# Kernel tuning notes

Measured on AMD Instinct MI355X. Metric: run time of the kernel, lower is better.

Reference implementation:

```python
import jax, jax.numpy as jnp
import numpy as np

B, SC, SV = 32, 300, 300
D, H, L, E, F = 512, 8, 6, 6, 1024
SEM = 768
VF = SEM + 1 + 1 + 6  # semantic + scene_offset + motion + emotion(6) = 776
CHORD, ROOT, ATTR = 159, 14, 14


def _ln(x, g, b, eps=1e-5):
    m = x.mean(-1, keepdims=True)
    v = ((x - m) ** 2).mean(-1, keepdims=True)
    return (x - m) / jnp.sqrt(v + eps) * g + b


def _mha(q_in, kv_in, qkv_w, qkv_b, ow, ob, mask=None):
    d = q_in.shape[-1]
    hd = d // H
    q = (q_in @ qkv_w[:d].T + qkv_b[:d]).reshape(q_in.shape[0], q_in.shape[1], H, hd)
    k = (kv_in @ qkv_w[d:2 * d].T + qkv_b[d:2 * d]).reshape(kv_in.shape[0], kv_in.shape[1], H, hd)
    v = (kv_in @ qkv_w[2 * d:].T + qkv_b[2 * d:]).reshape(kv_in.shape[0], kv_in.shape[1], H, hd)
    s = jnp.einsum('bqhd,bkhd->bhqk', q, k) / jnp.sqrt(jnp.asarray(hd, q.dtype))
    if mask is not None:
        s = s + mask
    a = jax.nn.softmax(s, axis=-1)
    o = jnp.einsum('bhqk,bkhd->bqhd', a, v).reshape(q_in.shape)
    return o @ ow.T + ob


def _moe(x, gw, gb, w1, b1, w2, b2, w3, b3):
    # top-2 routing over E experts, SwiGLU experts (GLUExpert)
    probs = jax.nn.softmax(x @ gw.T + gb, axis=-1)  # [B,S,E]
    topv, topi = jax.lax.top_k(probs, 2)
    wts = topv / topv.sum(-1, keepdims=True)
    full = (jax.nn.one_hot(topi, E, dtype=x.dtype) * wts[..., None]).sum(-2)  # [B,S,E]
    h = jax.nn.silu(jnp.einsum('bsd,edf->bsef', x, w1) + b1) * (jnp.einsum('bsd,edf->bsef', x, w2) + b2)
    eo = jnp.einsum('bsef,efd->bsed', h, w3) + b3
    return jnp.einsum('bse,bsed->bsd', full, eo)


def reference(x, x_root, x_attr, fsem, fkey, fscene, fmotion, femotion, emb_root, emb_attr, w_chord, b_chord, w_vis, b_vis, pos_c, pos_v, enc_qkv_w, enc_qkv_b, enc_ow, enc_ob, enc_ln1_g, enc_ln1_b, enc_ln2_g, enc_ln2_b, enc_gw, enc_gb, enc_w1, enc_b1, enc_w2, enc_b2, enc_w3, enc_b3, enc_fg, enc_fb, dec_sqkv_w, dec_sqkv_b, dec_sow, dec_sob, dec_cqkv_w, dec_cqkv_b, dec_cow, dec_cob, dec_ln1_g, dec_ln1_b, dec_ln2_g, dec_ln2_b, dec_ln3_g, dec_ln3_b, dec_gw, dec_gb, dec_w1, dec_b1, dec_w2, dec_b2, dec_w3, dec_b3, dec_fg, dec_fb, wout, bout):
    Bq, S = x_root.shape
    xe = emb_root[x_root] + emb_attr[x_attr]  # chord root + attr embeddings
    keyp = jnp.broadcast_to(fkey[:, 0][:, None, None], (Bq, S, 1)).astype(xe.dtype)
    xf = jnp.concatenate([xe, keyp], -1) @ w_chord.T + b_chord
    vfc = jnp.concatenate([fsem, fscene[..., None], fmotion[..., None], femotion], -1)  # [B,Sv,VF]
    vf = vfc @ w_vis.T + b_vis
    xf = xf + pos_c[:S][None]
    vf = vf + pos_v[:vf.shape[1]][None]
    causal = jnp.where(jnp.tril(jnp.ones((S, S), bool)), 0.0, jnp.finfo(xf.dtype).min).astype(xf.dtype)
    # encoder (post-norm): self-attn -> add&norm -> MoE -> add&norm
    h = vf
    for i in range(L):
        a = _mha(h, h, enc_qkv_w[i], enc_qkv_b[i], enc_ow[i], enc_ob[i])
        h = _ln(h + a, enc_ln1_g[i], enc_ln1_b[i])
        m = _moe(h, enc_gw[i], enc_gb[i], enc_w1[i], enc_b1[i], enc_w2[i], enc_b2[i], enc_w3[i], enc_b3[i])
        h = _ln(h + m, enc_ln2_g[i], enc_ln2_b[i])
    mem = _ln(h, enc_fg, enc_fb)
    # decoder: masked self-attn, cross-attn, MoE, each add&norm
    h = xf
    for i in range(L):
        a = _mha(h, h, dec_sqkv_w[i], dec_sqkv_b[i], dec_sow[i], dec_sob[i], causal)
        h = _ln(h + a, dec_ln1_g[i], dec_ln1_b[i])
        c = _mha(h, mem, dec_cqkv_w[i], dec_cqkv_b[i], dec_cow[i], dec_cob[i])
        h = _ln(h + c, dec_ln2_g[i], dec_ln2_b[i])
        m = _moe(h, dec_gw[i], dec_gb[i], dec_w1[i], dec_b1[i], dec_w2[i], dec_b2[i], dec_w3[i], dec_b3[i])
        h = _ln(h + m, dec_ln3_g[i], dec_ln3_b[i])
    h = _ln(h, dec_fg, dec_fb)
    return h @ wout.T + bout


def setup_inputs():
    key = jax.random.key(0)
    ks = iter(jax.random.split(key, 256))
    def nrm(*s):
        return jax.random.normal(next(ks), s, jnp.float32) * 0.02
    d = {}
    d['x'] = jax.random.randint(next(ks), (B, SC), 0, CHORD)
    d['x_root'] = jax.random.randint(next(ks), (B, SC), 0, ROOT)
    d['x_attr'] = jax.random.randint(next(ks), (B, SC), 0, ATTR)
    d['fsem'] = jax.random.normal(next(ks), (B, SV, SEM), jnp.float32)
    d['fkey'] = jax.random.uniform(next(ks), (B, 1), jnp.float32)
    d['fscene'] = jax.random.uniform(next(ks), (B, SV), jnp.float32)
    d['fmotion'] = jax.random.uniform(next(ks), (B, SV), jnp.float32)
    d['femotion'] = jax.random.uniform(next(ks), (B, SV, 6), jnp.float32)
    d['emb_root'] = nrm(ROOT, D)
    d['emb_attr'] = nrm(ATTR, D)
    d['w_chord'] = nrm(D, D + 1)
    d['b_chord'] = jnp.zeros((D,), jnp.float32)
    d['w_vis'] = nrm(D, VF)
    d['b_vis'] = jnp.zeros((D,), jnp.float32)
    d['pos_c'] = nrm(SC, D)
    d['pos_v'] = nrm(SV, D)
    def attn_params(pfx_qkv, pfx_o):
        d[pfx_qkv + '_w'] = nrm(L, 3 * D, D)
        d[pfx_qkv + '_b'] = jnp.zeros((L, 3 * D), jnp.float32)
        d[pfx_o + 'w'] = nrm(L, D, D)
        d[pfx_o + 'b'] = jnp.zeros((L, D), jnp.float32)
    attn_params('enc_qkv', 'enc_o')
    attn_params('dec_sqkv', 'dec_so')
    attn_params('dec_cqkv', 'dec_co')
    def moe_params(pfx):
        d[pfx + 'gw'] = nrm(L, E, D)
        d[pfx + 'gb'] = jnp.zeros((L, E), jnp.float32)
        d[pfx + 'w1'] = nrm(L, E, D, F)
        d[pfx + 'b1'] = jnp.zeros((L, E, F), jnp.float32)
        d[pfx + 'w2'] = nrm(L, E, D, F)
        d[pfx + 'b2'] = jnp.zeros((L, E, F), jnp.float32)
        d[pfx + 'w3'] = nrm(L, E, F, D)
        d[pfx + 'b3'] = jnp.zeros((L, E, D), jnp.float32)
    moe_params('enc_')
    moe_params('dec_')
    for n in ['enc_ln1', 'enc_ln2', 'dec_ln1', 'dec_ln2', 'dec_ln3']:
        d[n + '_g'] = jnp.ones((L, D), jnp.float32)
        d[n + '_b'] = jnp.zeros((L, D), jnp.float32)
    d['enc_fg'] = jnp.ones((D,), jnp.float32)
    d['enc_fb'] = jnp.zeros((D,), jnp.float32)
    d['dec_fg'] = jnp.ones((D,), jnp.float32)
    d['dec_fb'] = jnp.zeros((D,), jnp.float32)
    d['wout'] = nrm(CHORD, D)
    d['bout'] = jnp.zeros((CHORD,), jnp.float32)
    return d
```

## Files before the change

### kernel.cpp

```cpp
#include <hip/hip_runtime.h>

constexpr int B_ = 32, S_ = 300, D_ = 512, H_ = 8;
constexpr int L_ = 6, E_ = 6, F_ = 1024;
constexpr int CHORD_ = 159;
constexpr int R_ = B_ * S_;
constexpr int TD_ = 3 * D_;
constexpr int MT_ = R_ / 64;
constexpr size_t WSCAP_ = (size_t)E_ * F_ * 512;

typedef short bfrag __attribute__((ext_vector_type(8)));
typedef float facc  __attribute__((ext_vector_type(4)));

static __device__ __forceinline__ facc mfma_(bfrag a, bfrag b, facc c) {
    return __builtin_amdgcn_mfma_f32_16x16x32_bf16(a, b, c, 0, 0, 0);
}

static __device__ __forceinline__ short f2bf_rne(float f) {
    unsigned u = __float_as_uint(f);
    return (short)((u + 0x7FFFu + ((u >> 16) & 1u)) >> 16);
}
static __device__ __forceinline__ void split2(float x, short& hi, short& lo) {
    unsigned u = __float_as_uint(x);
    hi = (short)(u >> 16);
    float fh = __uint_as_float(u & 0xFFFF0000u);
    lo = f2bf_rne(x - fh);
}

static __device__ __forceinline__ float2 blockReduce2(float s, float ss) {
    __shared__ float red[4][2];
    #pragma unroll
    for (int o = 32; o > 0; o >>= 1) { s += __shfl_down(s, o); ss += __shfl_down(ss, o); }
    const int wid = threadIdx.x >> 6, lane = threadIdx.x & 63;
    if (lane == 0) { red[wid][0] = s; red[wid][1] = ss; }
    __syncthreads();
    if (threadIdx.x == 0) {
        for (int w = 1; w < 4; ++w) { s += red[w][0]; ss += red[w][1]; }
        red[0][0] = s; red[0][1] = ss;
    }
    __syncthreads();
    return make_float2(red[0][0], red[0][1]);
}

__global__ void wsplit_kern(const float* __restrict__ src, short* __restrict__ dh, short* __restrict__ dl,
                            int N, int K, int Kp)
{
    const int idx = blockIdx.x * 256 + threadIdx.x;
    if (idx >= N * Kp) return;
    const int n = idx / Kp, k = idx - n * Kp;
    const float v = (k < K) ? src[(size_t)n * K + k] : 0.f;
    short sh, sl; split2(v, sh, sl);
    dh[idx] = sh; dl[idx] = sl;
}

__global__ __launch_bounds__(256) void tsplit_kern(const float* __restrict__ src,
                                                   short* __restrict__ dh, short* __restrict__ dl,
                                                   int K, int N)
{
    __shared__ float tile[32][33];
    const size_t eo = (size_t)blockIdx.z * K * N;
    const float* s = src + eo;
    short* oh = dh + eo;
    short* ol = dl + eo;
    const int kb = blockIdx.x * 32, nb = blockIdx.y * 32;
    const int c = threadIdx.x & 31, r0 = threadIdx.x >> 5;
    #pragma unroll
    for (int p = 0; p < 4; ++p) {
        const int r = r0 + p * 8;
        tile[r][c] = s[(size_t)(kb + r) * N + nb + c];
    }
    __syncthreads();
    #pragma unroll
    for (int p = 0; p < 4; ++p) {
        const int wn = r0 + p * 8;
        const float v = tile[c][wn];
        short sh, sl; split2(v, sh, sl);
        const size_t o = (size_t)(nb + wn) * K + kb + c;
        oh[o] = sh; ol[o] = sl;
    }
}

__global__ __launch_bounds__(128) void gemm_mfma(
    const short* __restrict__ Xh, const short* __restrict__ Xl,
    const short* __restrict__ Wh, const short* __restrict__ Wl, int Kp,
    const float* __restrict__ bias, const float* __restrict__ pos,
    float* __restrict__ Y, int ldy, int N,
    short* __restrict__ Yh, short* __restrict__ Yl)
{
    __shared__ __align__(16) short Ah[64][40], Al[64][40];
    __shared__ __align__(16) short Bh[128][40], Bl[128][40];
    const int m0 = blockIdx.x * 64, n0 = blockIdx.y * 128;
    const int tid = threadIdx.x;
    const int w = tid >> 6, l = tid & 63;
    const facc zero = {0.f, 0.f, 0.f, 0.f};
    facc acc[4][4];
    #pragma unroll
    for (int i = 0; i < 4; ++i)
        #pragma unroll
        for (int j = 0; j < 4; ++j) acc[i][j] = zero;
    const int ar = tid >> 2, aks = (tid & 3) * 8;
    const int bcol = tid;
    const bool bok = (n0 + bcol) < N;
    const size_t bbase = (size_t)(n0 + bcol) * Kp;
    const bfrag zf = {0, 0, 0, 0, 0, 0, 0, 0};
    for (int kc = 0; kc < Kp; kc += 32) {
        #pragma unroll
        for (int p = 0; p < 2; ++p) {
            const int row = ar + p * 32;
            const size_t go = (size_t)(m0 + row) * Kp + kc + aks;
            *(bfrag*)&Ah[row][aks] = *(const bfrag*)&Xh[go];
            *(bfrag*)&Al[row][aks] = *(const bfrag*)&Xl[go];
        }
        if (bok) {
            #pragma unroll
            for (int i2 = 0; i2 < 4; ++i2) {
                *(bfrag*)&Bh[bcol][i2 * 8] = *(const bfrag*)&Wh[bbase + kc + i2 * 8];
                *(bfrag*)&Bl[bcol][i2 * 8] = *(const bfrag*)&Wl[bbase + kc + i2 * 8];
            }
        } else {
            #pragma unroll
            for (int i2 = 0; i2 < 4; ++i2) {
                *(bfrag*)&Bh[bcol][i2 * 8] = zf;
                *(bfrag*)&Bl[bcol][i2 * 8] = zf;
            }
        }
        __syncthreads();
        bfrag ah[4], al[4];
        #pragma unroll
        for (int i2 = 0; i2 < 4; ++i2) {
            ah[i2] = *(const bfrag*)&Ah[i2 * 16 + (l & 15)][(l >> 4) * 8];
            al[i2] = *(const bfrag*)&Al[i2 * 16 + (l & 15)][(l >> 4) * 8];
        }
        #pragma unroll
        for (int j = 0; j < 4; ++j) {
            const int cc = w * 64 + j * 16 + (l & 15);
            const bfrag bh = *(const bfrag*)&Bh[cc][(l >> 4) * 8];
            const bfrag bl = *(const bfrag*)&Bl[cc][(l >> 4) * 8];
            #pragma unroll
            for (int i2 = 0; i2 < 4; ++i2) {
                acc[i2][j] = mfma_(ah[i2], bh, acc[i2][j]);
                acc[i2][j] = mfma_(al[i2], bh, acc[i2][j]);
                acc[i2][j] = mfma_(ah[i2], bl, acc[i2][j]);
            }
        }
        __syncthreads();
    }
    #pragma unroll
    for (int i2 = 0; i2 < 4; ++i2) {
        #pragma unroll
        for (int r = 0; r < 4; ++r) {
            const int m = m0 + i2 * 16 + (l >> 4) * 4 + r;
            #pragma unroll
            for (int j = 0; j < 4; ++j) {
                const int n = n0 + w * 64 + j * 16 + (l & 15);
                if (n < N) {
                    float y = acc[i2][j][r];
                    if (bias) y += bias[n];
                    if (pos)  y += pos[(size_t)(m % S_) * N + n];
                    Y[(size_t)m * ldy + n] = y;
                    if (Yh) {
                        short sh, sl; split2(y, sh, sl);
                        Yh[(size_t)m * ldy + n] = sh;
                        Yl[(size_t)m * ldy + n] = sl;
                    }
                }
            }
        }
    }
}

template<bool CAUSAL>
__global__ __launch_bounds__(320) void attn_kern(const float* __restrict__ qkv,
                                                 short* __restrict__ oh, short* __restrict__ ol)
{
    __shared__ float Ks[64][64];
    __shared__ float Vs[64][64];
    const int b = blockIdx.x >> 3, hh = blockIdx.x & 7;
    const int tid = threadIdx.x;
    const float* base = qkv + (size_t)b * S_ * TD_ + hh * 64;
    const bool act = tid < S_;
    float4 q4[16];
    if (act) {
        const float4* qp = (const float4*)(base + (size_t)tid * TD_);
        #pragma unroll
        for (int dd = 0; dd < 16; ++dd) q4[dd] = qp[dd];
    }
    float m = -3.0e38f, lsum = 0.f;
    float acc[64];
    #pragma unroll
    for (int d = 0; d < 64; ++d) acc[d] = 0.f;
    for (int j0 = 0; j0 < S_; j0 += 64) {
        const int tn = min(64, S_ - j0);
        __syncthreads();
        for (int idx = tid; idx < 64 * 64; idx += 320) {
            const int jj = idx >> 6, d = idx & 63;
            const bool ok = jj < tn;
            Ks[jj][d] = ok ? base[(size_t)(j0 + jj) * TD_ + D_ + d] : 0.f;
            Vs[jj][d] = ok ? base[(size_t)(j0 + jj) * TD_ + 2 * D_ + d] : 0.f;
        }
        __syncthreads();
        if (act) {
            const int jmax = CAUSAL ? min(tn, tid - j0 + 1) : tn;
            for (int jj = 0; jj < jmax; ++jj) {
                const float4* kp = (const float4*)Ks[jj];
                float s = 0.f;
                #pragma unroll
                for (int dd = 0; dd < 16; ++dd) {
                    const float4 kv = kp[dd];
                    s += q4[dd].x * kv.x + q4[dd].y * kv.y + q4[dd].z * kv.z + q4[dd].w * kv.w;
                }
                s *= 0.125f;
                float p;
                if (s > m) {
                    const float r = __expf(m - s);
                    lsum *= r;
                    #pragma unroll
                    for (int d = 0; d < 64; ++d) acc[d] *= r;
                    m = s; p = 1.f;
                } else {
                    p = __expf(s - m);
                }
                lsum += p;
                const float4* vp = (const float4*)Vs[jj];
                #pragma unroll
                for (int dd = 0; dd < 16; ++dd) {
                    const float4 vv = vp[dd];
                    acc[dd * 4 + 0] += p * vv.x; acc[dd * 4 + 1] += p * vv.y;
                    acc[dd * 4 + 2] += p * vv.z; acc[dd * 4 + 3] += p * vv.w;
                }
            }
        }
    }
    if (act) {
        const float inv = 1.f / lsum;
        const size_t ob = (size_t)(b * S_ + tid) * D_ + hh * 64;
        #pragma unroll
        for (int d = 0; d < 64; ++d) {
            short sh, sl; split2(acc[d] * inv, sh, sl);
            oh[ob + d] = sh; ol[ob + d] = sl;
        }
    }
}

__global__ __launch_bounds__(256) void add_ln_kern(float* __restrict__ h, const float* __restrict__ a,
    const float* __restrict__ g, const float* __restrict__ bb,
    short* __restrict__ dh, short* __restrict__ dl)
{
    const int r = blockIdx.x, tid = threadIdx.x;
    const size_t off = (size_t)r * D_;
    const float x0 = h[off + tid] + a[off + tid];
    const float x1 = h[off + tid + 256] + a[off + tid + 256];
    const float2 red = blockReduce2(x0 + x1, x0 * x0 + x1 * x1);
    const float mean = red.x * (1.f / D_);
    const float var = red.y * (1.f / D_) - mean * mean;
    const float rs = rsqrtf(var + 1e-5f);
    const float y0 = (x0 - mean) * rs * g[tid] + bb[tid];
    const float y1 = (x1 - mean) * rs * g[tid + 256] + bb[tid + 256];
    h[off + tid] = y0; h[off + tid + 256] = y1;
    short sh, sl;
    split2(y0, sh, sl); dh[off + tid] = sh;       dl[off + tid] = sl;
    split2(y1, sh, sl); dh[off + tid + 256] = sh; dl[off + tid + 256] = sl;
}

__global__ __launch_bounds__(256) void add2_ln_kern(float* __restrict__ h, const float* __restrict__ moeout,
    const float* __restrict__ g, const float* __restrict__ bb,
    short* __restrict__ dh, short* __restrict__ dl)
{
    const int r = blockIdx.x, tid = threadIdx.x;
    const size_t off = (size_t)r * D_;
    const size_t m0 = (size_t)(2 * r) * D_, m1 = (size_t)(2 * r + 1) * D_;
    const float x0 = h[off + tid]       + moeout[m0 + tid]       + moeout[m1 + tid];
    const float x1 = h[off + tid + 256] + moeout[m0 + tid + 256] + moeout[m1 + tid + 256];
    const float2 red = blockReduce2(x0 + x1, x0 * x0 + x1 * x1);
    const float mean = red.x * (1.f / D_);
    const float var = red.y * (1.f / D_) - mean * mean;
    const float rs = rsqrtf(var + 1e-5f);
    const float y0 = (x0 - mean) * rs * g[tid] + bb[tid];
    const float y1 = (x1 - mean) * rs * g[tid + 256] + bb[tid + 256];
    h[off + tid] = y0; h[off + tid + 256] = y1;
    short sh, sl;
    split2(y0, sh, sl); dh[off + tid] = sh;       dl[off + tid] = sl;
    split2(y1, sh, sl); dh[off + tid + 256] = sh; dl[off + tid + 256] = sl;
}

__global__ __launch_bounds__(256) void ln_kern(const float* __restrict__ src,
    const float* __restrict__ g, const float* __restrict__ bb,
    short* __restrict__ dh, short* __restrict__ dl)
{
    const int r = blockIdx.x, tid = threadIdx.x;
    const size_t off = (size_t)r * D_;
    const float x0 = src[off + tid];
    const float x1 = src[off + tid + 256];
    const float2 red = blockReduce2(x0 + x1, x0 * x0 + x1 * x1);
    const float mean = red.x * (1.f / D_);
    const float var = red.y * (1.f / D_) - mean * mean;
    const float rs = rsqrtf(var + 1e-5f);
    const float y0 = (x0 - mean) * rs * g[tid] + bb[tid];
    const float y1 = (x1 - mean) * rs * g[tid + 256] + bb[tid + 256];
    short sh, sl;
    split2(y0, sh, sl); dh[off + tid] = sh;       dl[off + tid] = sl;
    split2(y1, sh, sl); dh[off + tid + 256] = sh; dl[off + tid + 256] = sl;
}

__global__ void assemble_chord_split(const int* __restrict__ x_root, const int* __restrict__ x_attr,
    const float* __restrict__ emb_root, const float* __restrict__ emb_attr,
    const float* __restrict__ fkey, short* __restrict__ dh, short* __restrict__ dl)
{
    const int idx = blockIdx.x * 256 + threadIdx.x;
    if (idx >= R_ * 544) return;
    const int r = idx / 544, k = idx - r * 544;
    float v = 0.f;
    if (k < D_)       v = emb_root[x_root[r] * D_ + k] + emb_attr[x_attr[r] * D_ + k];
    else if (k == D_) v = fkey[r / S_];
    short sh, sl; split2(v, sh, sl);
    dh[idx] = sh; dl[idx] = sl;
}

__global__ void assemble_vis_split(const float* __restrict__ fsem, const float* __restrict__ fscene,
    const float* __restrict__ fmotion, const float* __restrict__ femotion,
    short* __restrict__ dh, short* __restrict__ dl)
{
    const int idx = blockIdx.x * 256 + threadIdx.x;
    if (idx >= R_ * 800) return;
    const int r = idx / 800, k = idx - r * 800;
    float v = 0.f;
    if (k < 768)       v = fsem[(size_t)r * 768 + k];
    else if (k == 768) v = fscene[r];
    else if (k == 769) v = fmotion[r];
    else if (k < 776)  v = femotion[(size_t)r * 6 + (k - 770)];
    short sh, sl; split2(v, sh, sl);
    dh[idx] = sh; dl[idx] = sl;
}

__global__ __launch_bounds__(256) void moe_route(const float* __restrict__ X,
    const float* __restrict__ gw, const float* __restrict__ gb,
    int* __restrict__ gcnt, int* __restrict__ gtok, float* __restrict__ gwt)
{
    const int t = blockIdx.x * 256 + threadIdx.x;
    if (t >= R_) return;
    float lg[E_];
    #pragma unroll
    for (int e = 0; e < E_; ++e) lg[e] = gb[e];
    const float* xp = X + (size_t)t * D_;
    for (int d = 0; d < D_; ++d) {
        const float xd = xp[d];
        #pragma unroll
        for (int e = 0; e < E_; ++e) lg[e] += xd * gw[e * D_ + d];
    }
    float mx = lg[0];
    #pragma unroll
    for (int e = 1; e < E_; ++e) mx = fmaxf(mx, lg[e]);
    float p[E_];
    #pragma unroll
    for (int e = 0; e < E_; ++e) p[e] = __expf(lg[e] - mx);
    int i1 = 0;
    #pragma unroll
    for (int e = 1; e < E_; ++e) if (p[e] > p[i1]) i1 = e;
    int i2 = (i1 == 0) ? 1 : 0;
    #pragma unroll
    for (int e = 0; e < E_; ++e) if (e != i1 && p[e] > p[i2]) i2 = e;
    const float denom = p[i1] + p[i2];
    const float w1 = p[i1] / denom, w2 = p[i2] / denom;
    int pos1 = atomicAdd(&gcnt[i1], 1);
    gtok[i1 * R_ + pos1] = t * 2;     gwt[i1 * R_ + pos1] = w1;
    int pos2 = atomicAdd(&gcnt[i2], 1);
    gtok[i2 * R_ + pos2] = t * 2 + 1; gwt[i2 * R_ + pos2] = w2;
}

__global__ __launch_bounds__(128) void moe_stageA(
    const short* __restrict__ Xh, const short* __restrict__ Xl,
    const short* __restrict__ W1h, const short* __restrict__ W1l,
    const short* __restrict__ W2h, const short* __restrict__ W2l,
    const float* __restrict__ b1, const float* __restrict__ b2,
    const int* __restrict__ gcnt, const int* __restrict__ gtok,
    short* __restrict__ H1h, short* __restrict__ H1l)
{
    const int e = blockIdx.x / MT_, mt = blockIdx.x % MT_;
    const int cnt = gcnt[e];
    const int m0t = mt * 64;
    if (m0t >= cnt) return;
    __shared__ int rid[64];
    __shared__ __align__(16) short Ah[64][40], Al[64][40];
    __shared__ __align__(16) short B1h[64][40], B1l[64][40], B2h[64][40], B2l[64][40];
    const int tid = threadIdx.x;
    if (tid < 64) rid[tid] = (m0t + tid < cnt) ? gtok[e * R_ + m0t + tid] : -1;
    __syncthreads();
    const int f0 = blockIdx.y * 64;
    const int w = tid >> 6, l = tid & 63;
    const facc zero = {0.f, 0.f, 0.f, 0.f};
    facc acc1[4][2], acc2[4][2];
    #pragma unroll
    for (int i = 0; i < 4; ++i)
        #pragma unroll
        for (int j = 0; j < 2; ++j) { acc1[i][j] = zero; acc2[i][j] = zero; }
    const short* sh_ = (w == 0) ? (W1h + ((size_t)e * F_ + f0) * 512) : (W2h + ((size_t)e * F_ + f0) * 512);
    const short* sl_ = (w == 0) ? (W1l + ((size_t)e * F_ + f0) * 512) : (W2l + ((size_t)e * F_ + f0) * 512);
    short (*dsth)[40] = (w == 0) ? B1h : B2h;
    short (*dstl)[40] = (w == 0) ? B1l : B2l;
    const int ar = tid >> 2, aks = (tid & 3) * 8;
    const bfrag zf = {0, 0, 0, 0, 0, 0, 0, 0};
    for (int kc = 0; kc < 512; kc += 32) {
        #pragma unroll
        for (int p = 0; p < 2; ++p) {
            const int row = ar + p * 32;
            const int rr = rid[row];
            if (rr >= 0) {
                const size_t go = (size_t)(rr >> 1) * 512 + kc + aks;
                *(bfrag*)&Ah[row][aks] = *(const bfrag*)&Xh[go];
                *(bfrag*)&Al[row][aks] = *(const bfrag*)&Xl[go];
            } else {
                *(bfrag*)&Ah[row][aks] = zf;
                *(bfrag*)&Al[row][aks] = zf;
            }
        }
        {
            const size_t gb = (size_t)l * 512 + kc;
            #pragma unroll
            for (int i2 = 0; i2 < 4; ++i2) {
                *(bfrag*)&dsth[l][i2 * 8] = *(const bfrag*)&sh_[gb + i2 * 8];
                *(bfrag*)&dstl[l][i2 * 8] = *(const bfrag*)&sl_[gb + i2 * 8];
            }
        }
        __syncthreads();
        bfrag ah[4], al[4];
        #pragma unroll
        for (int i2 = 0; i2 < 4; ++i2) {
            ah[i2] = *(const bfrag*)&Ah[i2 * 16 + (l & 15)][(l >> 4) * 8];
            al[i2] = *(const bfrag*)&Al[i2 * 16 + (l & 15)][(l >> 4) * 8];
        }
        #pragma unroll
        for (int j = 0; j < 2; ++j) {
            const int cc = w * 32 + j * 16 + (l & 15);
            const bfrag b1hf = *(const bfrag*)&B1h[cc][(l >> 4) * 8];
            const bfrag b1lf = *(const bfrag*)&B1l[cc][(l >> 4) * 8];
            const bfrag b2hf = *(const bfrag*)&B2h[cc][(l >> 4) * 8];
            const bfrag b2lf = *(const bfrag*)&B2l[cc][(l >> 4) * 8];
            #pragma unroll
            for (int i2 = 0; i2 < 4; ++i2) {
                acc1[i2][j] = mfma_(ah[i2], b1hf, acc1[i2][j]);
                acc1[i2][j] = mfma_(al[i2], b1hf, acc1[i2][j]);
                acc1[i2][j] = mfma_(ah[i2], b1lf, acc1[i2][j]);
                acc2[i2][j] = mfma_(ah[i2], b2hf, acc2[i2][j]);
                acc2[i2][j] = mfma_(al[i2], b2hf, acc2[i2][j]);
                acc2[i2][j] = mfma_(ah[i2], b2lf, acc2[i2][j]);
            }
        }
        __syncthreads();
    }
    #pragma unroll
    for (int i2 = 0; i2 < 4; ++i2) {
        #pragma unroll
        for (int r = 0; r < 4; ++r) {
            const int mi = i2 * 16 + (l >> 4) * 4 + r;
            const int rr = rid[mi];
            if (rr < 0) continue;
            #pragma unroll
            for (int j = 0; j < 2; ++j) {
                const int f = f0 + w * 32 + j * 16 + (l & 15);
                const float a1 = acc1[i2][j][r] + b1[e * F_ + f];
                const float a2 = acc2[i2][j][r] + b2[e * F_ + f];
                const float hv = (a1 / (1.f + __expf(-a1))) * a2;
                const size_t oi = (size_t)rr * F_ + f;
                short hs, ls; split2(hv, hs, ls);
                H1h[oi] = hs; H1l[oi] = ls;
            }
        }
    }
}

__global__ __launch_bounds__(128) void moe_stageB(
    const short* __restrict__ Xh, const short* __restrict__ Xl,
    const short* __restrict__ W3h, const short* __restrict__ W3l,
    const float* __restrict__ b3,
    const int* __restrict__ gcnt, const int* __restrict__ gtok, const float* __restrict__ gwt,
    float* __restrict__ moeout)
{
    const int e = blockIdx.x / MT_, mt = blockIdx.x % MT_;
    const int cnt = gcnt[e];
    const int m0t = mt * 64;
    if (m0t >= cnt) return;
    __shared__ int rid[64];
    __shared__ float wts[64];
    __shared__ __align__(16) short Ah[64][40], Al[64][40];
    __shared__ __align__(16) short Bh[128][40], Bl[128][40];
    const int tid = threadIdx.x;
    if (tid < 64) {
        rid[tid] = (m0t + tid < cnt) ? gtok[e * R_ + m0t + tid] : -1;
        wts[tid] = (m0t + tid < cnt) ? gwt[e * R_ + m0t + tid] : 0.f;
    }
    __syncthreads();
    const int n0 = blockIdx.y * 128;
    const int w = tid >> 6, l = tid & 63;
    const facc zero = {0.f, 0.f, 0.f, 0.f};
    facc acc[4][4];
    #pragma unroll
    for (int i = 0; i < 4; ++i)
        #pragma unroll
        for (int j = 0; j < 4; ++j) acc[i][j] = zero;
    const int ar = tid >> 2, aks = (tid & 3) * 8;
    const int bcol = tid;
    const size_t bbase = ((size_t)e * 512 + n0 + bcol) * 1024;
    const bfrag zf = {0, 0, 0, 0, 0, 0, 0, 0};
    for (int kc = 0; kc < 1024; kc += 32) {
        #pragma unroll
        for (int p = 0; p < 2; ++p) {
            const int row = ar + p * 32;
            const int rr = rid[row];
            if (rr >= 0) {
                const size_t go = (size_t)rr * F_ + kc + aks;
                *(bfrag*)&Ah[row][aks] = *(const bfrag*)&Xh[go];
                *(bfrag*)&Al[row][aks] = *(const bfrag*)&Xl[go];
            } else {
                *(bfrag*)&Ah[row][aks] = zf;
                *(bfrag*)&Al[row][aks] = zf;
            }
        }
        #pragma unroll
        for (int i2 = 0; i2 < 4; ++i2) {
            *(bfrag*)&Bh[bcol][i2 * 8] = *(const bfrag*)&W3h[bbase + kc + i2 * 8];
            *(bfrag*)&Bl[bcol][i2 * 8] = *(const bfrag*)&W3l[bbase + kc + i2 * 8];
        }
        __syncthreads();
        bfrag ah[4], al[4];
        #pragma unroll
        for (int i2 = 0; i2 < 4; ++i2) {
            ah[i2] = *(const bfrag*)&Ah[i2 * 16 + (l & 15)][(l >> 4) * 8];
            al[i2] = *(const bfrag*)&Al[i2 * 16 + (l & 15)][(l >> 4) * 8];
        }
        #pragma unroll
        for (int j = 0; j < 4; ++j) {
            const int cc = w * 64 + j * 16 + (l & 15);
            const bfrag bh = *(const bfrag*)&Bh[cc][(l >> 4) * 8];
            const bfrag bl = *(const bfrag*)&Bl[cc][(l >> 4) * 8];
            #pragma unroll
            for (int i2 = 0; i2 < 4; ++i2) {
                acc[i2][j] = mfma_(ah[i2], bh, acc[i2][j]);
                acc[i2][j] = mfma_(al[i2], bh, acc[i2][j]);
                acc[i2][j] = mfma_(ah[i2], bl, acc[i2][j]);
            }
        }
        __syncthreads();
    }
    #pragma unroll
    for (int i2 = 0; i2 < 4; ++i2) {
        #pragma unroll
        for (int r = 0; r < 4; ++r) {
            const int mi = i2 * 16 + (l >> 4) * 4 + r;
            const int rr = rid[mi];
            if (rr < 0) continue;
            const float wt = wts[mi];
            #pragma unroll
            for (int j = 0; j < 4; ++j) {
                const int n = n0 + w * 64 + j * 16 + (l & 15);
                moeout[(size_t)rr * D_ + n] = wt * (acc[i2][j][r] + b3[e * D_ + n]);
            }
        }
    }
}

extern "C" void kernel_launch(void* const* d_in, const int* in_sizes, int n_in,
                              void* d_out, int out_size, void* d_ws, size_t ws_size,
                              hipStream_t stream) {
    (void)in_sizes; (void)n_in; (void)out_size; (void)ws_size;
    const int*   x_root    = (const int*)  d_in[1];
    const int*   x_attr    = (const int*)  d_in[2];
    const float* fsem      = (const float*)d_in[3];
    const float* fkey      = (const float*)d_in[4];
    const float* fscene    = (const float*)d_in[5];
    const float* fmotion   = (const float*)d_in[6];
    const float* femotion  = (const float*)d_in[7];
    const float* emb_root  = (const float*)d_in[8];
    const float* emb_attr  = (const float*)d_in[9];
    const float* w_chord   = (const float*)d_in[10];
    const float* b_chord   = (const float*)d_in[11];
    const float* w_vis     = (const float*)d_in[12];
    const float* b_vis     = (const float*)d_in[13];
    const float* pos_c     = (const float*)d_in[14];
    const float* pos_v     = (const float*)d_in[15];
    const float* enc_qkv_w = (const float*)d_in[16];
    const float* enc_qkv_b = (const float*)d_in[17];
    const float* enc_ow    = (const float*)d_in[18];
    const float* enc_ob    = (const float*)d_in[19];
    const float* dec_sqkv_w= (const float*)d_in[20];
    const float* dec_sqkv_b= (const float*)d_in[21];
    const float* dec_sow   = (const float*)d_in[22];
    const float* dec_sob   = (const float*)d_in[23];
    const float* dec_cqkv_w= (const float*)d_in[24];
    const float* dec_cqkv_b= (const float*)d_in[25];
    const float* dec_cow   = (const float*)d_in[26];
    const float* dec_cob   = (const float*)d_in[27];
    const float* enc_gw    = (const float*)d_in[28];
    const float* enc_gb    = (const float*)d_in[29];
    const float* enc_w1    = (const float*)d_in[30];
    const float* enc_b1    = (const float*)d_in[31];
    const float* enc_w2    = (const float*)d_in[32];
    const float* enc_b2    = (const float*)d_in[33];
    const float* enc_w3    = (const float*)d_in[34];
    const float* enc_b3    = (const float*)d_in[35];
    const float* dec_gw    = (const float*)d_in[36];
    const float* dec_gb    = (const float*)d_in[37];
    const float* dec_w1    = (const float*)d_in[38];
    const float* dec_b1    = (const float*)d_in[39];
    const float* dec_w2    = (const float*)d_in[40];
    const float* dec_b2    = (const float*)d_in[41];
    const float* dec_w3    = (const float*)d_in[42];
    const float* dec_b3    = (const float*)d_in[43];
    const float* enc_ln1_g = (const float*)d_in[44];
    const float* enc_ln1_b = (const float*)d_in[45];
    const float* enc_ln2_g = (const float*)d_in[46];
    const float* enc_ln2_b = (const float*)d_in[47];
    const float* dec_ln1_g = (const float*)d_in[48];
    const float* dec_ln1_b = (const float*)d_in[49];
    const float* dec_ln2_g = (const float*)d_in[50];
    const float* dec_ln2_b = (const float*)d_in[51];
    const float* dec_ln3_g = (const float*)d_in[52];
    const float* dec_ln3_b = (const float*)d_in[53];
    const float* enc_fg    = (const float*)d_in[54];
    const float* enc_fb    = (const float*)d_in[55];
    const float* dec_fg    = (const float*)d_in[56];
    const float* dec_fb    = (const float*)d_in[57];
    const float* wout      = (const float*)d_in[58];
    const float* bout      = (const float*)d_in[59];

    float* h    = (float*)d_ws;
    float* qkvb = h + (size_t)R_ * D_;
    short* PH   = (short*)(qkvb + (size_t)R_ * TD_);
    short* PL   = PH + (size_t)R_ * D_;
    short* MH   = PL + (size_t)R_ * D_;
    short* ML   = MH + (size_t)R_ * D_;
    short* H1H  = ML + (size_t)R_ * D_;
    short* H1L  = H1H + (size_t)2 * R_ * F_;
    short* WS0H = H1L + (size_t)2 * R_ * F_;
    short* WS0L = WS0H + WSCAP_;
    short* WS1H = WS0L + WSCAP_;
    short* WS1L = WS1H + WSCAP_;
    int*   gcnt = (int*)(WS1L + WSCAP_);
    int*   gtok = gcnt + 16;
    float* gwt  = (float*)(gtok + E_ * R_);
    short* AH   = (short*)qkvb;
    short* AL   = AH + (size_t)R_ * 800;

    auto wsplit = [&](const float* src, short* dh, short* dl, int N, int K, int Kp) {
        const int total = N * Kp;
        wsplit_kern<<<dim3((total + 255) / 256), dim3(256), 0, stream>>>(src, dh, dl, N, K, Kp);
    };
    auto tsplit = [&](const float* src, short* dh, short* dl, int K, int N) {
        tsplit_kern<<<dim3(K / 32, N / 32, E_), dim3(256), 0, stream>>>(src, dh, dl, K, N);
    };
    auto gemm = [&](const short* XhP, const short* XlP, int Kp,
                    const short* WhP, const short* WlP,
                    const float* bias, const float* pos,
                    float* Yf, int ldy, int N, short* Yh, short* Yl) {
        gemm_mfma<<<dim3(R_ / 64, (N + 127) / 128), dim3(128), 0, stream>>>(
            XhP, XlP, WhP, WlP, Kp, bias, pos, Yf, ldy, N, Yh, Yl);
    };
    auto run_moe = [&](const float* gw, const float* gb,
                       const float* w1, const float* b1, const float* w2, const float* b2,
                       const float* w3, const float* b3, const float* lng, const float* lnb) {
        hipMemsetAsync(gcnt, 0, 16 * sizeof(int), stream);
        moe_route<<<dim3((R_ + 255) / 256), dim3(256), 0, stream>>>(h, gw, gb, gcnt, gtok, gwt);
        tsplit(w1, WS0H, WS0L, D_, F_);
        tsplit(w2, WS1H, WS1L, D_, F_);
        moe_stageA<<<dim3(E_ * MT_, F_ / 64), dim3(128), 0, stream>>>(
            PH, PL, WS0H, WS0L, WS1H, WS1L, b1, b2, gcnt, gtok, H1H, H1L);
        tsplit(w3, WS0H, WS0L, F_, D_);
        moe_stageB<<<dim3(E_ * MT_, D_ / 128), dim3(128), 0, stream>>>(
            H1H, H1L, WS0H, WS0L, b3, gcnt, gtok, gwt, qkvb);
        add2_ln_kern<<<dim3(R_), dim3(256), 0, stream>>>(h, qkvb, lng, lnb, PH, PL);
    };

    wsplit(w_vis, WS0H, WS0L, D_, 776, 800);
    assemble_vis_split<<<dim3((R_ * 800 + 255) / 256), dim3(256), 0, stream>>>(
        fsem, fscene, fmotion, femotion, AH, AL);
    gemm(AH, AL, 800, WS0H, WS0L, b_vis, pos_v, h, D_, D_, PH, PL);

    for (int i = 0; i < L_; ++i) {
        wsplit(enc_qkv_w + (size_t)i * TD_ * D_, WS0H, WS0L, TD_, D_, D_);
        gemm(PH, PL, D_, WS0H, WS0L, enc_qkv_b + (size_t)i * TD_, nullptr, qkvb, TD_, TD_, nullptr, nullptr);
        attn_kern<false><<<dim3(B_ * H_), dim3(320), 0, stream>>>(qkvb, PH, PL);
        wsplit(enc_ow + (size_t)i * D_ * D_, WS0H, WS0L, D_, D_, D_);
        gemm(PH, PL, D_, WS0H, WS0L, enc_ob + (size_t)i * D_, nullptr, qkvb, D_, D_, nullptr, nullptr);
        add_ln_kern<<<dim3(R_), dim3(256), 0, stream>>>(h, qkvb, enc_ln1_g + i * D_, enc_ln1_b + i * D_, PH, PL);
        run_moe(enc_gw + (size_t)i * E_ * D_, enc_gb + (size_t)i * E_,
                enc_w1 + (size_t)i * E_ * D_ * F_, enc_b1 + (size_t)i * E_ * F_,
                enc_w2 + (size_t)i * E_ * D_ * F_, enc_b2 + (size_t)i * E_ * F_,
                enc_w3 + (size_t)i * E_ * F_ * D_, enc_b3 + (size_t)i * E_ * D_,
                enc_ln2_g + i * D_, enc_ln2_b + i * D_);
    }
    ln_kern<<<dim3(R_), dim3(256), 0, stream>>>(h, enc_fg, enc_fb, MH, ML);

    wsplit(w_chord, WS0H, WS0L, D_, 513, 544);
    assemble_chord_split<<<dim3((R_ * 544 + 255) / 256), dim3(256), 0, stream>>>(
        x_root, x_attr, emb_root, emb_attr, fkey, AH, AL);
    gemm(AH, AL, 544, WS0H, WS0L, b_chord, pos_c, h, D_, D_, PH, PL);

    for (int i = 0; i < L_; ++i) {
        wsplit(dec_sqkv_w + (size_t)i * TD_ * D_, WS0H, WS0L, TD_, D_, D_);
        gemm(PH, PL, D_, WS0H, WS0L, dec_sqkv_b + (size_t)i * TD_, nullptr, qkvb, TD_, TD_, nullptr, nullptr);
        attn_kern<true><<<dim3(B_ * H_), dim3(320), 0, stream>>>(qkvb, PH, PL);
        wsplit(dec_sow + (size_t)i * D_ * D_, WS0H, WS0L, D_, D_, D_);
        gemm(PH, PL, D_, WS0H, WS0L, dec_sob + (size_t)i * D_, nullptr, qkvb, D_, D_, nullptr, nullptr);
        add_ln_kern<<<dim3(R_), dim3(256), 0, stream>>>(h, qkvb, dec_ln1_g + i * D_, dec_ln1_b + i * D_, PH, PL);
        wsplit(dec_cqkv_w + (size_t)i * TD_ * D_, WS0H, WS0L, TD_, D_, D_);
        gemm(PH, PL, D_, WS0H, WS0L, dec_cqkv_b + (size_t)i * TD_, nullptr, qkvb, TD_, D_, nullptr, nullptr);
        gemm(MH, ML, D_, WS0H + (size_t)D_ * D_, WS0L + (size_t)D_ * D_,
             dec_cqkv_b + (size_t)i * TD_ + D_, nullptr, qkvb + D_, TD_, 2 * D_, nullptr, nullptr);
        attn_kern<false><<<dim3(B_ * H_), dim3(320), 0, stream>>>(qkvb, PH, PL);
        wsplit(dec_cow + (size_t)i * D_ * D_, WS0H, WS0L, D_, D_, D_);
        gemm(PH, PL, D_, WS0H, WS0L, dec_cob + (size_t)i * D_, nullptr, qkvb, D_, D_, nullptr, nullptr);
        add_ln_kern<<<dim3(R_), dim3(256), 0, stream>>>(h, qkvb, dec_ln2_g + i * D_, dec_ln2_b + i * D_, PH, PL);
        run_moe(dec_gw + (size_t)i * E_ * D_, dec_gb + (size_t)i * E_,
                dec_w1 + (size_t)i * E_ * D_ * F_, dec_b1 + (size_t)i * E_ * F_,
                dec_w2 + (size_t)i * E_ * D_ * F_, dec_b2 + (size_t)i * E_ * F_,
                dec_w3 + (size_t)i * E_ * F_ * D_, dec_b3 + (size_t)i * E_ * D_,
                dec_ln3_g + i * D_, dec_ln3_b + i * D_);
    }

    ln_kern<<<dim3(R_), dim3(256), 0, stream>>>(h, dec_fg, dec_fb, PH, PL);
    wsplit(wout, WS0H, WS0L, CHORD_, D_, D_);
    gemm(PH, PL, D_, WS0H, WS0L, bout, nullptr, (float*)d_out, CHORD_, CHORD_, nullptr, nullptr);
}
```

Baseline: 15.51 ms.

## Enlarge GEMM M-tiles to 128 with 4 waves and register-prefetch next K-chunk

The dense GEMM and both MoE expert GEMM stages move from 64-row to 128-row tiles with 256 threads (4 waves in a 2x2 layout), so each weight tile staged in shared memory is reused across twice as many rows. The global loads for the next K-chunk are now issued into registers right after the barrier and overlap the MFMA work on the current chunk, a simple software pipeline. R_=9600 divides by 128, so the dense GEMM grid stays exact. In exchange, register pressure and LDS use per block go up, and MoE tiles with few routed tokens waste more padded rows.

```diff
diff --git a/kernel.cpp b/kernel.cpp
--- a/kernel.cpp
+++ b/kernel.cpp
@@ -5,7 +5,7 @@
 constexpr int CHORD_ = 159;
 constexpr int R_ = B_ * S_;
 constexpr int TD_ = 3 * D_;
-constexpr int MT_ = R_ / 64;
+constexpr int MT2_ = R_ / 128;
 constexpr size_t WSCAP_ = (size_t)E_ * F_ * 512;
 
 typedef short bfrag __attribute__((ext_vector_type(8)));
@@ -79,18 +79,19 @@
     }
 }
 
-__global__ __launch_bounds__(128) void gemm_mfma(
+__global__ __launch_bounds__(256) void gemm_mfma(
     const short* __restrict__ Xh, const short* __restrict__ Xl,
     const short* __restrict__ Wh, const short* __restrict__ Wl, int Kp,
     const float* __restrict__ bias, const float* __restrict__ pos,
     float* __restrict__ Y, int ldy, int N,
     short* __restrict__ Yh, short* __restrict__ Yl)
 {
-    __shared__ __align__(16) short Ah[64][40], Al[64][40];
+    __shared__ __align__(16) short Ah[128][40], Al[128][40];
     __shared__ __align__(16) short Bh[128][40], Bl[128][40];
-    const int m0 = blockIdx.x * 64, n0 = blockIdx.y * 128;
+    const int m0 = blockIdx.x * 128, n0 = blockIdx.y * 128;
     const int tid = threadIdx.x;
     const int w = tid >> 6, l = tid & 63;
+    const int wr = (w >> 1) * 64, wc = (w & 1) * 64;
     const facc zero = {0.f, 0.f, 0.f, 0.f};
     facc acc[4][4];
     #pragma unroll
@@ -98,41 +99,42 @@
         #pragma unroll
         for (int j = 0; j < 4; ++j) acc[i][j] = zero;
     const int ar = tid >> 2, aks = (tid & 3) * 8;
-    const int bcol = tid;
-    const bool bok = (n0 + bcol) < N;
-    const size_t bbase = (size_t)(n0 + bcol) * Kp;
+    const int bc = tid >> 1, bk = (tid & 1) * 16;
+    const bool bok = (n0 + bc) < N;
+    const size_t a0 = (size_t)(m0 + ar) * Kp + aks;
+    const size_t a1 = a0 + (size_t)64 * Kp;
+    const size_t b0 = (size_t)(n0 + bc) * Kp + bk;
     const bfrag zf = {0, 0, 0, 0, 0, 0, 0, 0};
+    bfrag pa0h, pa0l, pa1h, pa1l, pb0h, pb0l, pb1h, pb1l;
+    auto LOAD = [&](int kc) {
+        pa0h = *(const bfrag*)&Xh[a0 + kc];
+        pa0l = *(const bfrag*)&Xl[a0 + kc];
+        pa1h = *(const bfrag*)&Xh[a1 + kc];
+        pa1l = *(const bfrag*)&Xl[a1 + kc];
+        if (bok) {
+            pb0h = *(const bfrag*)&Wh[b0 + kc];
+            pb0l = *(const bfrag*)&Wl[b0 + kc];
+            pb1h = *(const bfrag*)&Wh[b0 + kc + 8];
+            pb1l = *(const bfrag*)&Wl[b0 + kc + 8];
+        } else { pb0h = zf; pb0l = zf; pb1h = zf; pb1l = zf; }
+    };
+    LOAD(0);
     for (int kc = 0; kc < Kp; kc += 32) {
-        #pragma unroll
-        for (int p = 0; p < 2; ++p) {
-            const int row = ar + p * 32;
-            const size_t go = (size_t)(m0 + row) * Kp + kc + aks;
-            *(bfrag*)&Ah[row][aks] = *(const bfrag*)&Xh[go];
-            *(bfrag*)&Al[row][aks] = *(const bfrag*)&Xl[go];
-        }
-        if (bok) {
-            #pragma unroll
-            for (int i2 = 0; i2 < 4; ++i2) {
-                *(bfrag*)&Bh[bcol][i2 * 8] = *(const bfrag*)&Wh[bbase + kc + i2 * 8];
-                *(bfrag*)&Bl[bcol][i2 * 8] = *(const bfrag*)&Wl[bbase + kc + i2 * 8];
-            }
-        } else {
-            #pragma unroll
-            for (int i2 = 0; i2 < 4; ++i2) {
-                *(bfrag*)&Bh[bcol][i2 * 8] = zf;
-                *(bfrag*)&Bl[bcol][i2 * 8] = zf;
-            }
-        }
+        *(bfrag*)&Ah[ar][aks]      = pa0h;  *(bfrag*)&Al[ar][aks]      = pa0l;
+        *(bfrag*)&Ah[ar + 64][aks] = pa1h;  *(bfrag*)&Al[ar + 64][aks] = pa1l;
+        *(bfrag*)&Bh[bc][bk]       = pb0h;  *(bfrag*)&Bl[bc][bk]       = pb0l;
+        *(bfrag*)&Bh[bc][bk + 8]   = pb1h;  *(bfrag*)&Bl[bc][bk + 8]   = pb1l;
         __syncthreads();
+        if (kc + 32 < Kp) LOAD(kc + 32);
         bfrag ah[4], al[4];
         #pragma unroll
         for (int i2 = 0; i2 < 4; ++i2) {
-            ah[i2] = *(const bfrag*)&Ah[i2 * 16 + (l & 15)][(l >> 4) * 8];
-            al[i2] = *(const bfrag*)&Al[i2 * 16 + (l & 15)][(l >> 4) * 8];
+            ah[i2] = *(const bfrag*)&Ah[wr + i2 * 16 + (l & 15)][(l >> 4) * 8];
+            al[i2] = *(const bfrag*)&Al[wr + i2 * 16 + (l & 15)][(l >> 4) * 8];
         }
         #pragma unroll
         for (int j = 0; j < 4; ++j) {
-            const int cc = w * 64 + j * 16 + (l & 15);
+            const int cc = wc + j * 16 + (l & 15);
             const bfrag bh = *(const bfrag*)&Bh[cc][(l >> 4) * 8];
             const bfrag bl = *(const bfrag*)&Bl[cc][(l >> 4) * 8];
             #pragma unroll
@@ -148,10 +150,10 @@
     for (int i2 = 0; i2 < 4; ++i2) {
         #pragma unroll
         for (int r = 0; r < 4; ++r) {
-            const int m = m0 + i2 * 16 + (l >> 4) * 4 + r;
+            const int m = m0 + wr + i2 * 16 + (l >> 4) * 4 + r;
             #pragma unroll
             for (int j = 0; j < 4; ++j) {
-                const int n = n0 + w * 64 + j * 16 + (l & 15);
+                const int n = n0 + wc + j * 16 + (l & 15);
                 if (n < N) {
                     float y = acc[i2][j][r];
                     if (bias) y += bias[n];
@@ -366,7 +368,7 @@
     gtok[i2 * R_ + pos2] = t * 2 + 1; gwt[i2 * R_ + pos2] = w2;
 }
 
-__global__ __launch_bounds__(128) void moe_stageA(
+__global__ __launch_bounds__(256) void moe_stageA(
     const short* __restrict__ Xh, const short* __restrict__ Xl,
     const short* __restrict__ W1h, const short* __restrict__ W1l,
     const short* __restrict__ W2h, const short* __restrict__ W2l,
@@ -374,66 +376,66 @@
     const int* __restrict__ gcnt, const int* __restrict__ gtok,
     short* __restrict__ H1h, short* __restrict__ H1l)
 {
-    const int e = blockIdx.x / MT_, mt = blockIdx.x % MT_;
+    const int e = blockIdx.x / MT2_, mt = blockIdx.x % MT2_;
     const int cnt = gcnt[e];
-    const int m0t = mt * 64;
+    const int m0t = mt * 128;
     if (m0t >= cnt) return;
-    __shared__ int rid[64];
-    __shared__ __align__(16) short Ah[64][40], Al[64][40];
+    __shared__ int rid[128];
+    __shared__ __align__(16) short Ah[128][40], Al[128][40];
     __shared__ __align__(16) short B1h[64][40], B1l[64][40], B2h[64][40], B2l[64][40];
     const int tid = threadIdx.x;
-    if (tid < 64) rid[tid] = (m0t + tid < cnt) ? gtok[e * R_ + m0t + tid] : -1;
+    if (tid < 128) rid[tid] = (m0t + tid < cnt) ? gtok[e * R_ + m0t + tid] : -1;
     __syncthreads();
     const int f0 = blockIdx.y * 64;
     const int w = tid >> 6, l = tid & 63;
+    const int wr = (w >> 1) * 64, wf = (w & 1) * 32;
     const facc zero = {0.f, 0.f, 0.f, 0.f};
     facc acc1[4][2], acc2[4][2];
     #pragma unroll
     for (int i = 0; i < 4; ++i)
         #pragma unroll
         for (int j = 0; j < 2; ++j) { acc1[i][j] = zero; acc2[i][j] = zero; }
-    const short* sh_ = (w == 0) ? (W1h + ((size_t)e * F_ + f0) * 512) : (W2h + ((size_t)e * F_ + f0) * 512);
-    const short* sl_ = (w == 0) ? (W1l + ((size_t)e * F_ + f0) * 512) : (W2l + ((size_t)e * F_ + f0) * 512);
-    short (*dsth)[40] = (w == 0) ? B1h : B2h;
-    short (*dstl)[40] = (w == 0) ? B1l : B2l;
     const int ar = tid >> 2, aks = (tid & 3) * 8;
+    const int r0 = rid[ar], r1 = rid[ar + 64];
+    const size_t a0 = (r0 >= 0) ? ((size_t)(r0 >> 1) * 512 + aks) : 0;
+    const size_t a1 = (r1 >= 0) ? ((size_t)(r1 >> 1) * 512 + aks) : 0;
+    const int c = l;
+    const short* bsrc = (w == 0) ? W1h : (w == 1) ? W1l : (w == 2) ? W2h : W2l;
+    bsrc += ((size_t)e * F_ + f0 + c) * 512;
+    short (*bdst)[40] = (w == 0) ? B1h : (w == 1) ? B1l : (w == 2) ? B2h : B2l;
     const bfrag zf = {0, 0, 0, 0, 0, 0, 0, 0};
+    bfrag pa0h, pa0l, pa1h, pa1l, pb0, pb1, pb2, pb3;
+    auto LOAD = [&](int kc) {
+        pa0h = (r0 >= 0) ? *(const bfrag*)&Xh[a0 + kc] : zf;
+        pa0l = (r0 >= 0) ? *(const bfrag*)&Xl[a0 + kc] : zf;
+        pa1h = (r1 >= 0) ? *(const bfrag*)&Xh[a1 + kc] : zf;
+        pa1l = (r1 >= 0) ? *(const bfrag*)&Xl[a1 + kc] : zf;
+        pb0 = *(const bfrag*)&bsrc[kc];
+        pb1 = *(const bfrag*)&bsrc[kc + 8];
+        pb2 = *(const bfrag*)&bsrc[kc + 16];
+        pb3 = *(const bfrag*)&bsrc[kc + 24];
+    };
+    LOAD(0);
     for (int kc = 0; kc < 512; kc += 32) {
-        #pragma unroll
-        for (int p = 0; p < 2; ++p) {
-            const int row = ar + p * 32;
-            const int rr = rid[row];
-            if (rr >= 0) {
-                const size_t go = (size_t)(rr >> 1) * 512 + kc + aks;
-                *(bfrag*)&Ah[row][aks] = *(const bfrag*)&Xh[go];
-                *(bfrag*)&Al[row][aks] = *(const bfrag*)&Xl[go];
-            } else {
-                *(bfrag*)&Ah[row][aks] = zf;
-                *(bfrag*)&Al[row][aks] = zf;
-            }
-        }
-        {
-            const size_t gb = (size_t)l * 512 + kc;
-            #pragma unroll
-            for (int i2 = 0; i2 < 4; ++i2) {
-                *(bfrag*)&dsth[l][i2 * 8] = *(const bfrag*)&sh_[gb + i2 * 8];
-                *(bfrag*)&dstl[l][i2 * 8] = *(const bfrag*)&sl_[gb + i2 * 8];
-            }
-        }
+        *(bfrag*)&Ah[ar][aks]      = pa0h;  *(bfrag*)&Al[ar][aks]      = pa0l;
+        *(bfrag*)&Ah[ar + 64][aks] = pa1h;  *(bfrag*)&Al[ar + 64][aks] = pa1l;
+        *(bfrag*)&bdst[c][0]  = pb0;  *(bfrag*)&bdst[c][8]  = pb1;
+        *(bfrag*)&bdst[c][16] = pb2;  *(bfrag*)&bdst[c][24] = pb3;
         __syncthreads();
+        if (kc + 32 < 512) LOAD(kc + 32);
         bfrag ah[4], al[4];
         #pragma unroll
         for (int i2 = 0; i2 < 4; ++i2) {
-            ah[i2] = *(const bfrag*)&Ah[i2 * 16 + (l & 15)][(l >> 4) * 8];
-            al[i2] = *(const bfrag*)&Al[i2 * 16 + (l & 15)][(l >> 4) * 8];
+            ah[i2] = *(const bfrag*)&Ah[wr + i2 * 16 + (l & 15)][(l >> 4) * 8];
+            al[i2] = *(const bfrag*)&Al[wr + i2 * 16 + (l & 15)][(l >> 4) * 8];
         }
         #pragma unroll
         for (int j = 0; j < 2; ++j) {
-            const int cc = w * 32 + j * 16 + (l & 15);
-            const bfrag b1hf = *(const bfrag*)&B1h[cc][(l >> 4) * 8];
-            const bfrag b1lf = *(const bfrag*)&B1l[cc][(l >> 4) * 8];
-            const bfrag b2hf = *(const bfrag*)&B2h[cc][(l >> 4) * 8];
-            const bfrag b2lf = *(const bfrag*)&B2l[cc][(l >> 4) * 8];
+            const int fc = wf + j * 16 + (l & 15);
+            const bfrag b1hf = *(const bfrag*)&B1h[fc][(l >> 4) * 8];
+            const bfrag b1lf = *(const bfrag*)&B1l[fc][(l >> 4) * 8];
+            const bfrag b2hf = *(const bfrag*)&B2h[fc][(l >> 4) * 8];
+            const bfrag b2lf = *(const bfrag*)&B2l[fc][(l >> 4) * 8];
             #pragma unroll
             for (int i2 = 0; i2 < 4; ++i2) {
                 acc1[i2][j] = mfma_(ah[i2], b1hf, acc1[i2][j]);
@@ -450,15 +452,15 @@
     for (int i2 = 0; i2 < 4; ++i2) {
         #pragma unroll
         for (int r = 0; r < 4; ++r) {
-            const int mi = i2 * 16 + (l >> 4) * 4 + r;
+            const int mi = wr + i2 * 16 + (l >> 4) * 4 + r;
             const int rr = rid[mi];
             if (rr < 0) continue;
             #pragma unroll
             for (int j = 0; j < 2; ++j) {
-                const int f = f0 + w * 32 + j * 16 + (l & 15);
-                const float a1 = acc1[i2][j][r] + b1[e * F_ + f];
-                const float a2 = acc2[i2][j][r] + b2[e * F_ + f];
-                const float hv = (a1 / (1.f + __expf(-a1))) * a2;
+                const int f = f0 + wf + j * 16 + (l & 15);
+                const float a1v = acc1[i2][j][r] + b1[e * F_ + f];
+                const float a2v = acc2[i2][j][r] + b2[e * F_ + f];
+                const float hv = (a1v / (1.f + __expf(-a1v))) * a2v;
                 const size_t oi = (size_t)rr * F_ + f;
                 short hs, ls; split2(hv, hs, ls);
                 H1h[oi] = hs; H1l[oi] = ls;
@@ -467,29 +469,30 @@
     }
 }
 
-__global__ __launch_bounds__(128) void moe_stageB(
+__global__ __launch_bounds__(256) void moe_stageB(
     const short* __restrict__ Xh, const short* __restrict__ Xl,
     const short* __restrict__ W3h, const short* __restrict__ W3l,
     const float* __restrict__ b3,
     const int* __restrict__ gcnt, const int* __restrict__ gtok, const float* __restrict__ gwt,
     float* __restrict__ moeout)
 {
-    const int e = blockIdx.x / MT_, mt = blockIdx.x % MT_;
+    const int e = blockIdx.x / MT2_, mt = blockIdx.x % MT2_;
     const int cnt = gcnt[e];
-    const int m0t = mt * 64;
+    const int m0t = mt * 128;
     if (m0t >= cnt) return;
-    __shared__ int rid[64];
-    __shared__ float wts[64];
-    __shared__ __align__(16) short Ah[64][40], Al[64][40];
+    __shared__ int rid[128];
+    __shared__ float wts[128];
+    __shared__ __align__(16) short Ah[128][40], Al[128][40];
     __shared__ __align__(16) short Bh[128][40], Bl[128][40];
     const int tid = threadIdx.x;
-    if (tid < 64) {
+    if (tid < 128) {
         rid[tid] = (m0t + tid < cnt) ? gtok[e * R_ + m0t + tid] : -1;
         wts[tid] = (m0t + tid < cnt) ? gwt[e * R_ + m0t + tid] : 0.f;
     }
     __syncthreads();
     const int n0 = blockIdx.y * 128;
     const int w = tid >> 6, l = tid & 63;
+    const int wr = (w >> 1) * 64, wc = (w & 1) * 64;
     const facc zero = {0.f, 0.f, 0.f, 0.f};
     facc acc[4][4];
     #pragma unroll
@@ -497,38 +500,40 @@
         #pragma unroll
         for (int j = 0; j < 4; ++j) acc[i][j] = zero;
     const int ar = tid >> 2, aks = (tid & 3) * 8;
-    const int bcol = tid;
-    const size_t bbase = ((size_t)e * 512 + n0 + bcol) * 1024;
+    const int r0 = rid[ar], r1 = rid[ar + 64];
+    const size_t a0 = (r0 >= 0) ? ((size_t)r0 * F_ + aks) : 0;
+    const size_t a1 = (r1 >= 0) ? ((size_t)r1 * F_ + aks) : 0;
+    const int bc = tid >> 1, bk = (tid & 1) * 16;
+    const size_t b0 = ((size_t)e * 512 + n0 + bc) * 1024 + bk;
     const bfrag zf = {0, 0, 0, 0, 0, 0, 0, 0};
+    bfrag pa0h, pa0l, pa1h, pa1l, pb0h, pb0l, pb1h, pb1l;
+    auto LOAD = [&](int kc) {
+        pa0h = (r0 >= 0) ? *(const bfrag*)&Xh[a0 + kc] : zf;
+        pa0l = (r0 >= 0) ? *(const bfrag*)&Xl[a0 + kc] : zf;
+        pa1h = (r1 >= 0) ? *(const bfrag*)&Xh[a1 + kc] : zf;
+        pa1l = (r1 >= 0) ? *(const bfrag*)&Xl[a1 + kc] : zf;
+        pb0h = *(const bfrag*)&W3h[b0 + kc];
+        pb0l = *(const bfrag*)&W3l[b0 + kc];
+        pb1h = *(const bfrag*)&W3h[b0 + kc + 8];
+        pb1l = *(const bfrag*)&W3l[b0 + kc + 8];
+    };
+    LOAD(0);
     for (int kc = 0; kc < 1024; kc += 32) {
-        #pragma unroll
-        for (int p = 0; p < 2; ++p) {
-            const int row = ar + p * 32;
-            const int rr = rid[row];
-            if (rr >= 0) {
-                const size_t go = (size_t)rr * F_ + kc + aks;
-                *(bfrag*)&Ah[row][aks] = *(const bfrag*)&Xh[go];
-                *(bfrag*)&Al[row][aks] = *(const bfrag*)&Xl[go];
-            } else {
-                *(bfrag*)&Ah[row][aks] = zf;
-                *(bfrag*)&Al[row][aks] = zf;
-            }
-        }
+        *(bfrag*)&Ah[ar][aks]      = pa0h;  *(bfrag*)&Al[ar][aks]      = pa0l;
+        *(bfrag*)&Ah[ar + 64][aks] = pa1h;  *(bfrag*)&Al[ar + 64][aks] = pa1l;
+        *(bfrag*)&Bh[bc][bk]       = pb0h;  *(bfrag*)&Bl[bc][bk]       = pb0l;
+        *(bfrag*)&Bh[bc][bk + 8]   = pb1h;  *(bfrag*)&Bl[bc][bk + 8]   = pb1l;
+        __syncthreads();
+        if (kc + 32 < 1024) LOAD(kc + 32);
+        bfrag ah[4], al[4];
         #pragma unroll
         for (int i2 = 0; i2 < 4; ++i2) {
-            *(bfrag*)&Bh[bcol][i2 * 8] = *(const bfrag*)&W3h[bbase + kc + i2 * 8];
-            *(bfrag*)&Bl[bcol][i2 * 8] = *(const bfrag*)&W3l[bbase + kc + i2 * 8];
-        }
-        __syncthreads();
-        bfrag ah[4], al[4];
-        #pragma unroll
-        for (int i2 = 0; i2 < 4; ++i2) {
-            ah[i2] = *(const bfrag*)&Ah[i2 * 16 + (l & 15)][(l >> 4) * 8];
-            al[i2] = *(const bfrag*)&Al[i2 * 16 + (l & 15)][(l >> 4) * 8];
+            ah[i2] = *(const bfrag*)&Ah[wr + i2 * 16 + (l & 15)][(l >> 4) * 8];
+            al[i2] = *(const bfrag*)&Al[wr + i2 * 16 + (l & 15)][(l >> 4) * 8];
         }
         #pragma unroll
         for (int j = 0; j < 4; ++j) {
-            const int cc = w * 64 + j * 16 + (l & 15);
+            const int cc = wc + j * 16 + (l & 15);
             const bfrag bh = *(const bfrag*)&Bh[cc][(l >> 4) * 8];
             const bfrag bl = *(const bfrag*)&Bl[cc][(l >> 4) * 8];
             #pragma unroll
@@ -544,13 +549,13 @@
     for (int i2 = 0; i2 < 4; ++i2) {
         #pragma unroll
         for (int r = 0; r < 4; ++r) {
-            const int mi = i2 * 16 + (l >> 4) * 4 + r;
+            const int mi = wr + i2 * 16 + (l >> 4) * 4 + r;
             const int rr = rid[mi];
             if (rr < 0) continue;
             const float wt = wts[mi];
             #pragma unroll
             for (int j = 0; j < 4; ++j) {
-                const int n = n0 + w * 64 + j * 16 + (l & 15);
+                const int n = n0 + wc + j * 16 + (l & 15);
                 moeout[(size_t)rr * D_ + n] = wt * (acc[i2][j][r] + b3[e * D_ + n]);
             }
         }
@@ -650,7 +655,7 @@
                     const short* WhP, const short* WlP,
                     const float* bias, const float* pos,
                     float* Yf, int ldy, int N, short* Yh, short* Yl) {
-        gemm_mfma<<<dim3(R_ / 64, (N + 127) / 128), dim3(128), 0, stream>>>(
+        gemm_mfma<<<dim3(R_ / 128, (N + 127) / 128), dim3(256), 0, stream>>>(
             XhP, XlP, WhP, WlP, Kp, bias, pos, Yf, ldy, N, Yh, Yl);
     };
     auto run_moe = [&](const float* gw, const float* gb,
@@ -660,10 +665,10 @@
         moe_route<<<dim3((R_ + 255) / 256), dim3(256), 0, stream>>>(h, gw, gb, gcnt, gtok, gwt);
         tsplit(w1, WS0H, WS0L, D_, F_);
         tsplit(w2, WS1H, WS1L, D_, F_);
-        moe_stageA<<<dim3(E_ * MT_, F_ / 64), dim3(128), 0, stream>>>(
+        moe_stageA<<<dim3(E_ * MT2_, F_ / 64), dim3(256), 0, stream>>>(
             PH, PL, WS0H, WS0L, WS1H, WS1L, b1, b2, gcnt, gtok, H1H, H1L);
         tsplit(w3, WS0H, WS0L, F_, D_);
-        moe_stageB<<<dim3(E_ * MT_, D_ / 128), dim3(128), 0, stream>>>(
+        moe_stageB<<<dim3(E_ * MT2_, D_ / 128), dim3(256), 0, stream>>>(
             H1H, H1L, WS0H, WS0L, b3, gcnt, gtok, gwt, qkvb);
         add2_ln_kern<<<dim3(R_), dim3(256), 0, stream>>>(h, qkvb, lng, lnb, PH, PL);
     };
```

After: 12.81 ms. 17.4% less time.
